# Optimization experiments

Hardware: AMD Instinct MI355X
Metric: run time of the kernel (lower is better)

## Reference

```python
import jax, jax.numpy as jnp
import numpy as np

B, Q, K, D = 32, 1024, 1024, 64
MASK_VAL = -1000000.0  # matches torch source's -1e6 fill


def setup_inputs() -> dict:
    key = jax.random.key(0)
    kq, kk, kv, kl = jax.random.split(key, 4)
    return {
        "queries": jax.random.normal(kq, (B, Q, D), dtype=jnp.float32),
        "keys": jax.random.normal(kk, (B, K, D), dtype=jnp.float32),
        "values": jax.random.normal(kv, (B, K, D), dtype=jnp.float32),
        "valid_lens": jax.random.randint(kl, (B,), 1, K + 1, dtype=jnp.int64),
    }


def reference(queries, keys, values, valid_lens):
    d = queries.shape[-1]
    # [B, Q, K] scores
    scores = jnp.einsum("bqd,bkd->bqk", queries, keys) / jnp.sqrt(jnp.asarray(d, queries.dtype))
    # 1D valid_lens -> same length mask for every query row of a batch element
    kv_pos = jnp.arange(scores.shape[-1])  # [K]
    mask = kv_pos[None, None, :] < valid_lens[:, None, None]  # [B, 1, K] broadcast
    scores = jnp.where(mask, scores, MASK_VAL)
    attn = jax.nn.softmax(scores, axis=-1)
    # dropout p=0.0 -> identity
    return jnp.einsum("bqk,bkd->bqd", attn, values)
```

## Files before the change

### kernel.cpp

```cpp
#include <hip/hip_runtime.h>
#include <hip/hip_bf16.h>

#define NB 32
#define NQ 1024
#define NK 1024
#define ND 64
#define BK 64
#define M_FIX 16.0f

typedef __attribute__((ext_vector_type(8))) __bf16 bf16x8;
typedef __attribute__((ext_vector_type(8))) short  s16x8;
typedef __attribute__((ext_vector_type(4))) float  f32x4;

static __device__ __forceinline__ short f2bf(float f) {
  unsigned u = __builtin_bit_cast(unsigned, f);
  u += 0x7fffu + ((u >> 16) & 1u);
  return (short)(u >> 16);
}

static __device__ __forceinline__ int swzoff(int row, int gcol) {
  return row * 64 + (((gcol ^ (row & 7)) & 7) << 3);
}

#define GLD_LDS16(gp, lp)                                              \
  __builtin_amdgcn_global_load_lds(                                    \
      (const __attribute__((address_space(1))) void*)(gp),             \
      (__attribute__((address_space(3))) void*)(lp), 16, 0, 0)

__launch_bounds__(256)
__global__ void prep_kv(const float* __restrict__ Kp, const float* __restrict__ Vp,
                        const int* __restrict__ VLp,
                        short* __restrict__ Kb, short* __restrict__ Vt) {
  __shared__ __align__(16) short T[64 * 72];
  const int wg = blockIdx.x;
  const int b  = wg >> 4;
  const int kt = wg & 15;

  const bool is64 = (VLp[1] == 0);
  const int  len  = is64 ? VLp[2 * b] : VLp[b];
  if (kt * 64 >= len) return;

  const int tid = threadIdx.x;

  {
    const int key = tid >> 2, d0 = (tid & 3) * 16, g0 = (tid & 3) * 2;
    const float* src = Kp + ((size_t)(b * NK + kt * 64 + key)) * ND + d0;
    short out[16];
#pragma unroll
    for (int i = 0; i < 16; i += 4) {
      float4 v = *(const float4*)(src + i);
      out[i] = f2bf(v.x); out[i + 1] = f2bf(v.y);
      out[i + 2] = f2bf(v.z); out[i + 3] = f2bf(v.w);
    }
    short* dtile = Kb + ((size_t)(b * 16 + kt)) * 4096;
    *(s16x8*)&dtile[swzoff(key, g0)]     = *(const s16x8*)out;
    *(s16x8*)&dtile[swzoff(key, g0 + 1)] = *(const s16x8*)(out + 8);
  }

  {
    const int vkey = tid & 63, vd0 = (tid >> 6) * 16;
    const float* src = Vp + ((size_t)(b * NK + kt * 64 + vkey)) * ND + vd0;
#pragma unroll
    for (int i = 0; i < 4; ++i) {
      float4 v = *(const float4*)(src + i * 4);
      T[(vd0 + i * 4 + 0) * 72 + vkey] = f2bf(v.x);
      T[(vd0 + i * 4 + 1) * 72 + vkey] = f2bf(v.y);
      T[(vd0 + i * 4 + 2) * 72 + vkey] = f2bf(v.z);
      T[(vd0 + i * 4 + 3) * 72 + vkey] = f2bf(v.w);
    }
  }
  __syncthreads();
  {
    const int d = tid >> 2, c = (tid & 3) * 16, g0 = (tid & 3) * 2;
    short* vtile = Vt + ((size_t)(b * 16 + kt)) * 4096;
    *(s16x8*)&vtile[swzoff(d, g0)]     = *(const s16x8*)&T[d * 72 + c];
    *(s16x8*)&vtile[swzoff(d, g0 + 1)] = *(const s16x8*)&T[d * 72 + c + 8];
  }
}

__launch_bounds__(512, 4)
__global__ void attn_fwd(const float* __restrict__ Qp,
                         const short* __restrict__ Kb,
                         const short* __restrict__ Vt,
                         const int* __restrict__ VLp,
                         float* __restrict__ Op) {
  __shared__ __align__(16) short SM[40960];

  const int wg  = blockIdx.x;
  const int swz = (wg & 7) * 64 + (wg >> 3);
  const int b   = swz >> 4;
  const int qb  = swz & 15;

  const int tid  = threadIdx.x;
  const int wid  = tid >> 6;
  const int lane = tid & 63;
  const int l16  = lane & 15;
  const int grp  = lane >> 4;
  const int esw  = l16 & 7;
  const int qgrp = wid >> 1;
  const int par  = wid & 1;

  const bool is64 = (VLp[1] == 0);
  const int  len  = is64 ? VLp[2 * b] : VLp[b];
  const int  ntiles = (len + BK - 1) >> 6;
  const int  nsup   = (ntiles + 1) >> 1;
  const int  remLast = len - ((ntiles - 1) << 6);

  const float qscale = 0.125f * 1.44269504088896341f;

  bf16x8 qf[2];
  {
    const float* qsrc = Qp + ((size_t)(b * NQ + qb * 64 + qgrp * 16 + l16)) * ND + grp * 8;
#pragma unroll
    for (int k2 = 0; k2 < 2; ++k2) {
      float4 a = *(const float4*)(qsrc + k2 * 32);
      float4 c = *(const float4*)(qsrc + k2 * 32 + 4);
      s16x8 t;
      t[0] = f2bf(a.x * qscale); t[1] = f2bf(a.y * qscale);
      t[2] = f2bf(a.z * qscale); t[3] = f2bf(a.w * qscale);
      t[4] = f2bf(c.x * qscale); t[5] = f2bf(c.y * qscale);
      t[6] = f2bf(c.z * qscale); t[7] = f2bf(c.w * qscale);
      qf[k2] = __builtin_bit_cast(bf16x8, t);
    }
  }

  const short* kg = Kb + (size_t)b * 16 * 4096;
  const short* vg = Vt + (size_t)b * 16 * 4096;

  auto dma = [&](int buf, int t0) {
    GLD_LDS16(kg + (size_t)t0 * 4096 + tid * 8,       &SM[buf * 8192 + wid * 512]);
    GLD_LDS16(kg + (size_t)(t0 + 1) * 4096 + tid * 8, &SM[buf * 8192 + 4096 + wid * 512]);
    GLD_LDS16(vg + (size_t)t0 * 4096 + tid * 8,       &SM[16384 + buf * 8192 + wid * 512]);
    GLD_LDS16(vg + (size_t)(t0 + 1) * 4096 + tid * 8, &SM[16384 + buf * 8192 + 4096 + wid * 512]);
  };

  short* pw  = &SM[32768 + wid * 1024];
  int*   pwd = (int*)pw;
  int paddr[8];
#pragma unroll
  for (int n = 0; n < 4; ++n)
#pragma unroll
    for (int a = 0; a < 2; ++a)
      paddr[n * 2 + a] = l16 * 32 + (((2 * n + (grp >> 1)) ^ esw) << 2) + ((2 * grp + a) & 3);
  int prd[2];
#pragma unroll
  for (int ks = 0; ks < 2; ++ks)
    prd[ks] = l16 * 64 + (((4 * ks + grp) ^ esw) << 3);

  const f32x4 vzero = {0.f, 0.f, 0.f, 0.f};
  f32x4 oacc[4];
#pragma unroll
  for (int i = 0; i < 4; ++i) oacc[i] = vzero;
  float lrun = 0.f;

  dma(0, 0);
  int buf = 0;

  for (int it = 0; it < nsup; ++it) {
    if (it + 1 < nsup) {
      dma(buf ^ 1, 2 * (it + 1));
      asm volatile("s_waitcnt vmcnt(4)" ::: "memory");
    } else {
      asm volatile("s_waitcnt vmcnt(0)" ::: "memory");
    }
    __builtin_amdgcn_sched_barrier(0);
    __builtin_amdgcn_s_barrier();
    __builtin_amdgcn_sched_barrier(0);

    const int myt = 2 * it + par;
    if (myt < ntiles) {
      const short* kw = &SM[buf * 8192 + par * 4096];
      const short* vw = &SM[16384 + buf * 8192 + par * 4096];

      f32x4 sc[4];
      __builtin_amdgcn_s_setprio(1);
#pragma unroll
      for (int n = 0; n < 4; ++n) {
        f32x4 acc = vzero;
#pragma unroll
        for (int k2 = 0; k2 < 2; ++k2) {
          bf16x8 kf = __builtin_bit_cast(bf16x8,
              *(const s16x8*)&kw[swzoff(n * 16 + l16, k2 * 4 + grp)]);
          acc = __builtin_amdgcn_mfma_f32_16x16x32_bf16(kf, qf[k2], acc, 0, 0, 0);
        }
        sc[n] = acc;
      }
      __builtin_amdgcn_s_setprio(0);

      if (myt == ntiles - 1) {
#pragma unroll
        for (int n = 0; n < 4; ++n)
#pragma unroll
          for (int r = 0; r < 4; ++r) {
            float x = (n * 16 + grp * 4 + r < remLast) ? sc[n][r] - M_FIX : -128.0f;
            float pv = exp2f(x);
            sc[n][r] = pv;
            lrun += pv;
          }
      } else {
#pragma unroll
        for (int n = 0; n < 4; ++n)
#pragma unroll
          for (int r = 0; r < 4; ++r) {
            float pv = exp2f(sc[n][r] - M_FIX);
            sc[n][r] = pv;
            lrun += pv;
          }
      }

#pragma unroll
      for (int n = 0; n < 4; ++n)
#pragma unroll
        for (int a = 0; a < 2; ++a) {
          int d;
          asm("v_cvt_pk_bf16_f32 %0, %1, %2"
              : "=v"(d) : "v"(sc[n][2 * a]), "v"(sc[n][2 * a + 1]));
          pwd[paddr[n * 2 + a]] = d;
        }

      asm volatile("s_waitcnt lgkmcnt(0)" ::: "memory");
      __builtin_amdgcn_sched_barrier(0);

      bf16x8 pf[2];
#pragma unroll
      for (int ks = 0; ks < 2; ++ks)
        pf[ks] = __builtin_bit_cast(bf16x8, *(const s16x8*)&pw[prd[ks]]);

      __builtin_amdgcn_s_setprio(1);
#pragma unroll
      for (int nd = 0; nd < 4; ++nd) {
#pragma unroll
        for (int k2 = 0; k2 < 2; ++k2) {
          bf16x8 vf = __builtin_bit_cast(bf16x8,
              *(const s16x8*)&vw[swzoff(nd * 16 + l16, k2 * 4 + grp)]);
          oacc[nd] = __builtin_amdgcn_mfma_f32_16x16x32_bf16(pf[k2], vf, oacc[nd], 0, 0, 0);
        }
      }
      __builtin_amdgcn_s_setprio(0);
    }

    asm volatile("s_waitcnt lgkmcnt(0)" ::: "memory");
    __builtin_amdgcn_sched_barrier(0);
    __builtin_amdgcn_s_barrier();
    __builtin_amdgcn_sched_barrier(0);
    buf ^= 1;
  }

  __syncthreads();
  float* CB = (float*)SM;
  const int crow = qgrp * 64 + lane;
  if (par == 1) {
    float* dst = CB + (size_t)crow * 20;
#pragma unroll
    for (int nd = 0; nd < 4; ++nd) *(f32x4*)(dst + nd * 4) = oacc[nd];
    dst[16] = lrun;
  }
  __syncthreads();
  if (par == 0) {
    const float* src = CB + (size_t)crow * 20;
#pragma unroll
    for (int nd = 0; nd < 4; ++nd) oacc[nd] += *(const f32x4*)(src + nd * 4);
    float l = lrun + src[16];
    l += __shfl_xor(l, 16);
    l += __shfl_xor(l, 32);
    const float inv = 1.0f / l;
    float invr[4];
#pragma unroll
    for (int r = 0; r < 4; ++r)
      invr[r] = __shfl(inv, (lane & 48) | (grp * 4 + r));

    float* obase = Op + ((size_t)(b * NQ + qb * 64 + qgrp * 16)) * ND;
#pragma unroll
    for (int nd = 0; nd < 4; ++nd)
#pragma unroll
      for (int r = 0; r < 4; ++r)
        obase[(grp * 4 + r) * ND + nd * 16 + l16] = oacc[nd][r] * invr[r];
  }
}

extern "C" void kernel_launch(void* const* d_in, const int* in_sizes, int n_in,
                              void* d_out, int out_size, void* d_ws, size_t ws_size,
                              hipStream_t stream) {
  const float* Qp = (const float*)d_in[0];
  const float* Kp = (const float*)d_in[1];
  const float* Vp = (const float*)d_in[2];
  const int*   VL = (const int*)d_in[3];
  float* Op = (float*)d_out;

  short* Kb = (short*)d_ws;
  short* Vt = Kb + (size_t)NB * NK * ND;

  prep_kv<<<dim3(NB * 16), dim3(256), 0, stream>>>(Kp, Vp, VL, Kb, Vt);
  attn_fwd<<<dim3(NB * 16), dim3(512), 0, stream>>>(Qp, Kb, Vt, VL, Op);
}
```

Baseline: 30.57 us.

## Use a single barrier per iteration, prefetch after barrier, fold max offset into MFMA init

Restructures the double-buffered K/V loop to one barrier per iteration: wait for all loads, barrier, then issue the next tile's direct-to-LDS loads. The old trailing barrier is removed. It also precomputes byte-offset LDS addresses to cut per-iteration address arithmetic. The fixed softmax offset is folded into the MFMA accumulator's initial value, dropping a subtraction per score. The trade-off is that each iteration now waits on vmcnt(0), so load latency is overlapped only with the current tile's compute rather than a full iteration ahead.

Result: faster. 28.99 us (-5.2%).

```diff
diff --git a/kernel.cpp b/kernel.cpp
--- a/kernel.cpp
+++ b/kernel.cpp
@@ -85,6 +85,7 @@
                          const int* __restrict__ VLp,
                          float* __restrict__ Op) {
   __shared__ __align__(16) short SM[40960];
+  char* smb = (char*)SM;
 
   const int wg  = blockIdx.x;
   const int swz = (wg & 7) * 64 + (wg >> 3);
@@ -124,65 +125,65 @@
     }
   }
 
-  const short* kg = Kb + (size_t)b * 16 * 4096;
-  const short* vg = Vt + (size_t)b * 16 * 4096;
-
-  auto dma = [&](int buf, int t0) {
-    GLD_LDS16(kg + (size_t)t0 * 4096 + tid * 8,       &SM[buf * 8192 + wid * 512]);
-    GLD_LDS16(kg + (size_t)(t0 + 1) * 4096 + tid * 8, &SM[buf * 8192 + 4096 + wid * 512]);
-    GLD_LDS16(vg + (size_t)t0 * 4096 + tid * 8,       &SM[16384 + buf * 8192 + wid * 512]);
-    GLD_LDS16(vg + (size_t)(t0 + 1) * 4096 + tid * 8, &SM[16384 + buf * 8192 + 4096 + wid * 512]);
-  };
-
-  short* pw  = &SM[32768 + wid * 1024];
-  int*   pwd = (int*)pw;
-  int paddr[8];
+  int ka0 = par * 8192 + l16 * 128 + ((((0 * 4 + grp) ^ esw)) << 4);
+  int ka1 = par * 8192 + l16 * 128 + ((((1 * 4 + grp) ^ esw)) << 4);
+  int pra[2], pwa[8];
+#pragma unroll
+  for (int ks = 0; ks < 2; ++ks)
+    pra[ks] = 65536 + wid * 2048 + l16 * 128 + (((ks * 4 + grp) ^ esw) << 4);
 #pragma unroll
   for (int n = 0; n < 4; ++n)
 #pragma unroll
     for (int a = 0; a < 2; ++a)
-      paddr[n * 2 + a] = l16 * 32 + (((2 * n + (grp >> 1)) ^ esw) << 2) + ((2 * grp + a) & 3);
-  int prd[2];
-#pragma unroll
-  for (int ks = 0; ks < 2; ++ks)
-    prd[ks] = l16 * 64 + (((4 * ks + grp) ^ esw) << 3);
-
+      pwa[n * 2 + a] = 65536 + wid * 2048 + l16 * 128
+                     + ((((2 * n + (grp >> 1)) ^ esw)) << 4) + (((2 * grp + a) & 3) << 2);
+
+  const char* kgp = (const char*)(Kb + (size_t)b * 16 * 4096) + tid * 16;
+  const char* vgp = (const char*)(Vt + (size_t)b * 16 * 4096) + tid * 16;
+  const int dstW = wid * 1024;
+
+  const f32x4 minit = {-M_FIX, -M_FIX, -M_FIX, -M_FIX};
   const f32x4 vzero = {0.f, 0.f, 0.f, 0.f};
   f32x4 oacc[4];
 #pragma unroll
   for (int i = 0; i < 4; ++i) oacc[i] = vzero;
   float lrun = 0.f;
 
-  dma(0, 0);
-  int buf = 0;
+  int bufB = 0;
+
+  GLD_LDS16(kgp,        smb + dstW);
+  GLD_LDS16(kgp + 8192, smb + 8192 + dstW);
+  GLD_LDS16(vgp,        smb + 32768 + dstW);
+  GLD_LDS16(vgp + 8192, smb + 40960 + dstW);
+  kgp += 16384; vgp += 16384;
 
   for (int it = 0; it < nsup; ++it) {
-    if (it + 1 < nsup) {
-      dma(buf ^ 1, 2 * (it + 1));
-      asm volatile("s_waitcnt vmcnt(4)" ::: "memory");
-    } else {
-      asm volatile("s_waitcnt vmcnt(0)" ::: "memory");
-    }
+    asm volatile("s_waitcnt vmcnt(0)" ::: "memory");
     __builtin_amdgcn_sched_barrier(0);
     __builtin_amdgcn_s_barrier();
     __builtin_amdgcn_sched_barrier(0);
 
+    if (it + 1 < nsup) {
+      const int nb = bufB ^ 16384;
+      GLD_LDS16(kgp,        smb + nb + dstW);
+      GLD_LDS16(kgp + 8192, smb + nb + 8192 + dstW);
+      GLD_LDS16(vgp,        smb + 32768 + nb + dstW);
+      GLD_LDS16(vgp + 8192, smb + 32768 + nb + 8192 + dstW);
+      kgp += 16384; vgp += 16384;
+    }
+
     const int myt = 2 * it + par;
     if (myt < ntiles) {
-      const short* kw = &SM[buf * 8192 + par * 4096];
-      const short* vw = &SM[16384 + buf * 8192 + par * 4096];
-
       f32x4 sc[4];
       __builtin_amdgcn_s_setprio(1);
 #pragma unroll
       for (int n = 0; n < 4; ++n) {
-        f32x4 acc = vzero;
-#pragma unroll
-        for (int k2 = 0; k2 < 2; ++k2) {
-          bf16x8 kf = __builtin_bit_cast(bf16x8,
-              *(const s16x8*)&kw[swzoff(n * 16 + l16, k2 * 4 + grp)]);
-          acc = __builtin_amdgcn_mfma_f32_16x16x32_bf16(kf, qf[k2], acc, 0, 0, 0);
-        }
+        bf16x8 kf0 = __builtin_bit_cast(bf16x8,
+            *(const s16x8*)(smb + bufB + ka0 + n * 2048));
+        bf16x8 kf1 = __builtin_bit_cast(bf16x8,
+            *(const s16x8*)(smb + bufB + ka1 + n * 2048));
+        f32x4 acc = __builtin_amdgcn_mfma_f32_16x16x32_bf16(kf0, qf[0], minit, 0, 0, 0);
+        acc = __builtin_amdgcn_mfma_f32_16x16x32_bf16(kf1, qf[1], acc, 0, 0, 0);
         sc[n] = acc;
       }
       __builtin_amdgcn_s_setprio(0);
@@ -192,7 +193,7 @@
         for (int n = 0; n < 4; ++n)
 #pragma unroll
           for (int r = 0; r < 4; ++r) {
-            float x = (n * 16 + grp * 4 + r < remLast) ? sc[n][r] - M_FIX : -128.0f;
+            float x = (n * 16 + grp * 4 + r < remLast) ? sc[n][r] : -128.0f;
             float pv = exp2f(x);
             sc[n][r] = pv;
             lrun += pv;
@@ -202,7 +203,7 @@
         for (int n = 0; n < 4; ++n)
 #pragma unroll
           for (int r = 0; r < 4; ++r) {
-            float pv = exp2f(sc[n][r] - M_FIX);
+            float pv = exp2f(sc[n][r]);
             sc[n][r] = pv;
             lrun += pv;
           }
@@ -215,7 +216,7 @@
           int d;
           asm("v_cvt_pk_bf16_f32 %0, %1, %2"
               : "=v"(d) : "v"(sc[n][2 * a]), "v"(sc[n][2 * a + 1]));
-          pwd[paddr[n * 2 + a]] = d;
+          *(int*)(smb + pwa[n * 2 + a]) = d;
         }
 
       asm volatile("s_waitcnt lgkmcnt(0)" ::: "memory");
@@ -224,26 +225,22 @@
       bf16x8 pf[2];
 #pragma unroll
       for (int ks = 0; ks < 2; ++ks)
-        pf[ks] = __builtin_bit_cast(bf16x8, *(const s16x8*)&pw[prd[ks]]);
+        pf[ks] = __builtin_bit_cast(bf16x8, *(const s16x8*)(smb + pra[ks]));
 
       __builtin_amdgcn_s_setprio(1);
 #pragma unroll
       for (int nd = 0; nd < 4; ++nd) {
-#pragma unroll
-        for (int k2 = 0; k2 < 2; ++k2) {
-          bf16x8 vf = __builtin_bit_cast(bf16x8,
-              *(const s16x8*)&vw[swzoff(nd * 16 + l16, k2 * 4 + grp)]);
-          oacc[nd] = __builtin_amdgcn_mfma_f32_16x16x32_bf16(pf[k2], vf, oacc[nd], 0, 0, 0);
-        }
+        bf16x8 vf0 = __builtin_bit_cast(bf16x8,
+            *(const s16x8*)(smb + bufB + ka0 + 32768 + nd * 2048));
+        bf16x8 vf1 = __builtin_bit_cast(bf16x8,
+            *(const s16x8*)(smb + bufB + ka1 + 32768 + nd * 2048));
+        oacc[nd] = __builtin_amdgcn_mfma_f32_16x16x32_bf16(pf[0], vf0, oacc[nd], 0, 0, 0);
+        oacc[nd] = __builtin_amdgcn_mfma_f32_16x16x32_bf16(pf[1], vf1, oacc[nd], 0, 0, 0);
       }
       __builtin_amdgcn_s_setprio(0);
     }
 
-    asm volatile("s_waitcnt lgkmcnt(0)" ::: "memory");
-    __builtin_amdgcn_sched_barrier(0);
-    __builtin_amdgcn_s_barrier();
-    __builtin_amdgcn_sched_barrier(0);
-    buf ^= 1;
+    bufB ^= 16384;
   }
 
   __syncthreads();
```
